# Kernel tuning notes

Measured on AMD Instinct MI355X. Metric: run time of the kernel, lower is better.

## Reference

```python
import jax, jax.numpy as jnp
import numpy as np

N_HEAD = 16
N_FEAT = 1024
HEAD_DIM = N_FEAT // N_HEAD


def setup_inputs() -> dict:
    key = jax.random.key(0)
    ks = jax.random.split(key, 13)
    B, Tq, Tc = 2, 1024, 1024
    s = 0.02
    return {
        "query": jax.random.normal(ks[0], (B, Tq, N_FEAT), jnp.float32),
        "key": jax.random.normal(ks[1], (B, Tq, N_FEAT), jnp.float32),
        "value": jax.random.normal(ks[2], (B, Tq, N_FEAT), jnp.float32),
        "cache": jax.random.normal(ks[3], (B, N_HEAD, Tc, 2 * HEAD_DIM), jnp.float32),
        "Wq": jax.random.normal(ks[4], (N_FEAT, N_FEAT), jnp.float32) * s,
        "bq": jax.random.normal(ks[5], (N_FEAT,), jnp.float32) * s,
        "Wk": jax.random.normal(ks[6], (N_FEAT, N_FEAT), jnp.float32) * s,
        "bk": jax.random.normal(ks[7], (N_FEAT,), jnp.float32) * s,
        "Wv": jax.random.normal(ks[8], (N_FEAT, N_FEAT), jnp.float32) * s,
        "bv": jax.random.normal(ks[9], (N_FEAT,), jnp.float32) * s,
        "Wo": jax.random.normal(ks[10], (N_FEAT, N_FEAT), jnp.float32) * s,
        "bo": jax.random.normal(ks[11], (N_FEAT,), jnp.float32) * s,
    }


def _split_heads(x, B):
    # [B, T, C] -> [B, H, T, D]
    return x.reshape(B, -1, N_HEAD, HEAD_DIM).transpose(0, 2, 1, 3)


def reference(query, key, value, cache, Wq, bq, Wk, bk, Wv, bv, Wo, bo):
    B, Tq, _ = query.shape
    # torch Linear: y = x @ W.T + b
    q = _split_heads(query @ Wq.T + bq, B)   # [B,H,Tq,D]
    k = _split_heads(key @ Wk.T + bk, B)     # [B,H,Tk,D]
    v = _split_heads(value @ Wv.T + bv, B)
    # KV-cache concat (cache holds [K | V] along last dim)
    k_cache, v_cache = jnp.split(cache, 2, axis=-1)
    k = jnp.concatenate([k_cache, k], axis=2)
    v = jnp.concatenate([v_cache, v], axis=2)
    new_cache = jnp.concatenate([k, v], axis=-1)
    scores = jnp.einsum("bhqd,bhkd->bhqk", q, k) / np.sqrt(HEAD_DIM).astype(jnp.float32)
    attn = jax.nn.softmax(scores, axis=-1)  # fake mask path; dropout is identity (rate 0 / eval)
    x = jnp.einsum("bhqk,bhkd->bhqd", attn, v)
    x = x.transpose(0, 2, 1, 3).reshape(B, Tq, N_FEAT)
    out = x @ Wo.T + bo
    return out, new_cache
```

## Files before the change

kernel.cpp:

```cpp
#include <hip/hip_runtime.h>

typedef short short4s __attribute__((ext_vector_type(4)));
typedef short short8 __attribute__((ext_vector_type(8)));
typedef __bf16 bf16x8 __attribute__((ext_vector_type(8)));
typedef float f32x4 __attribute__((ext_vector_type(4)));

#define NFEAT 1024
#define HDIM  64
#define NHEAD 16
#define TC2   2048
#define QSCL  0.18033688011112043f

__device__ __forceinline__ short f2bf(float f) {
    unsigned int u = __builtin_bit_cast(unsigned int, f);
    u += 0x7fffu + ((u >> 16) & 1u);
    return (short)(u >> 16);
}
__device__ __forceinline__ short f2bfq(float f) {
    __bf16 h = (__bf16)f;
    return __builtin_bit_cast(short, h);
}

__device__ __forceinline__ f32x4 mfma_bf16(short8 a, short8 b, f32x4 c) {
    return __builtin_amdgcn_mfma_f32_16x16x32_bf16(
        __builtin_bit_cast(bf16x8, a), __builtin_bit_cast(bf16x8, b), c, 0, 0, 0);
}

#define GLOAD16(gp, lp) __builtin_amdgcn_global_load_lds( \
    (const __attribute__((address_space(1))) void*)(gp),  \
    (__attribute__((address_space(3))) void*)(lp), 16, 0, 0)

__global__ __launch_bounds__(256) void prep_kernel(
    const float* __restrict__ q, const float* __restrict__ k, const float* __restrict__ v,
    const float* __restrict__ Wq, const float* __restrict__ Wk,
    const float* __restrict__ Wv, const float* __restrict__ Wo,
    const float4* __restrict__ cache4,
    short* __restrict__ qin, short* __restrict__ kin, short* __restrict__ vin,
    short* __restrict__ wqb, short* __restrict__ wkb, short* __restrict__ wvb,
    short* __restrict__ wob,
    float4* __restrict__ nc4, short* __restrict__ kbb, short* __restrict__ vtb)
{
    const int b = blockIdx.x, tid = threadIdx.x;
    if (b < 5120) {
        const float* src; short* dst; size_t base;
        if (b < 1024)      { src = q;  dst = qin; base = (size_t)b * 2048; }
        else if (b < 2048) { src = k;  dst = kin; base = (size_t)(b - 1024) * 2048; }
        else if (b < 3072) { src = v;  dst = vin; base = (size_t)(b - 2048) * 2048; }
        else if (b < 3584) { src = Wq; dst = wqb; base = (size_t)(b - 3072) * 2048; }
        else if (b < 4096) { src = Wk; dst = wkb; base = (size_t)(b - 3584) * 2048; }
        else if (b < 4608) { src = Wv; dst = wvb; base = (size_t)(b - 4096) * 2048; }
        else               { src = Wo; dst = wob; base = (size_t)(b - 4608) * 2048; }
        size_t i = base + (size_t)tid * 8;
        float4 a0 = *(const float4*)(src + i);
        float4 a1 = *(const float4*)(src + i + 4);
        short8 o;
        o[0] = f2bf(a0.x); o[1] = f2bf(a0.y); o[2] = f2bf(a0.z); o[3] = f2bf(a0.w);
        o[4] = f2bf(a1.x); o[5] = f2bf(a1.y); o[6] = f2bf(a1.z); o[7] = f2bf(a1.w);
        *(short8*)(dst + i) = o;
    } else {
        int i = (b - 5120) * 256 + tid;
        int c4 = i & 31;
        int t  = (i >> 5) & 1023;
        int bh = i >> 15;
        float4 val = cache4[i];
        nc4[((size_t)bh * TC2 + t) * 32 + c4] = val;
        int c = c4 * 4;
        if (c < 64) {
            size_t base = ((size_t)bh * TC2 + t) * HDIM + c;
            kbb[base + 0] = f2bf(val.x); kbb[base + 1] = f2bf(val.y);
            kbb[base + 2] = f2bf(val.z); kbb[base + 3] = f2bf(val.w);
        } else {
            int d = c - 64;
            size_t base = ((size_t)bh * HDIM + d) * TC2 + t;
            vtb[base + 0 * TC2] = f2bf(val.x); vtb[base + 1 * TC2] = f2bf(val.y);
            vtb[base + 2 * TC2] = f2bf(val.z); vtb[base + 3 * TC2] = f2bf(val.w);
        }
    }
}

__global__ __launch_bounds__(256) void gemm128(
    const short* __restrict__ A0, const short* __restrict__ A1, const short* __restrict__ A2,
    const short* __restrict__ W0, const short* __restrict__ W1, const short* __restrict__ W2,
    const float* __restrict__ b0, const float* __restrict__ b1, const float* __restrict__ b2,
    float* __restrict__ outf, short* __restrict__ qbuf,
    short* __restrict__ kbb, short* __restrict__ vtb, int base_mode)
{
    __shared__ short As[128 * 64];
    __shared__ short Bs[128 * 64];

    int mode;
    const short *A, *W;
    const float* bias;
    if (base_mode == 3) { mode = 3; A = A0; W = W0; bias = b0; }
    else {
        mode = blockIdx.z;
        if (mode == 0)      { A = A0; W = W0; bias = b0; }
        else if (mode == 1) { A = A1; W = W1; bias = b1; }
        else                { A = A2; W = W2; bias = b2; }
    }

    const int tid = threadIdx.x, lane = tid & 63, w = tid >> 6;
    const int wr = w >> 1, wc = w & 1;
    const int lr = lane & 15, lg = lane >> 4;
    const int bx = blockIdx.x, by = blockIdx.y;

    f32x4 acc[4][4];
#pragma unroll
    for (int m = 0; m < 4; ++m)
#pragma unroll
        for (int n = 0; n < 4; ++n) acc[m][n] = (f32x4){0.f, 0.f, 0.f, 0.f};

    const short* agBase = A + (size_t)(by * 128 + w * 32 + (lane >> 3)) * 1024 + (lane & 7) * 8;
    const short* bgBase = W + (size_t)(bx * 128 + w * 32 + (lane >> 3)) * 1024 + (lane & 7) * 8;
    short* asW = &As[w * 2048];
    short* bsW = &Bs[w * 2048];

    for (int kt = 0; kt < 16; ++kt) {
        const short* ag = agBase + kt * 64;
        const short* bg = bgBase + kt * 64;
        GLOAD16(ag,          asW);
        GLOAD16(ag + 8192,   asW + 512);
        GLOAD16(ag + 16384,  asW + 1024);
        GLOAD16(ag + 24576,  asW + 1536);
        GLOAD16(bg,          bsW);
        GLOAD16(bg + 8192,   bsW + 512);
        GLOAD16(bg + 16384,  bsW + 1024);
        GLOAD16(bg + 24576,  bsW + 1536);
        __syncthreads();
#pragma unroll
        for (int kk = 0; kk < 2; ++kk) {
            short8 af[4], bf[4];
#pragma unroll
            for (int m = 0; m < 4; ++m)
                af[m] = *(const short8*)&As[(wr * 64 + m * 16 + lr) * 64 + kk * 32 + lg * 8];
#pragma unroll
            for (int n = 0; n < 4; ++n)
                bf[n] = *(const short8*)&Bs[(wc * 64 + n * 16 + lr) * 64 + kk * 32 + lg * 8];
#pragma unroll
            for (int m = 0; m < 4; ++m)
#pragma unroll
                for (int n = 0; n < 4; ++n)
                    acc[m][n] = mfma_bf16(af[m], bf[n], acc[m][n]);
        }
        __syncthreads();
    }

#pragma unroll
    for (int m = 0; m < 4; ++m) {
#pragma unroll
        for (int n = 0; n < 4; ++n) {
            const int cg = bx * 128 + wc * 64 + n * 16 + lr;
            const int rg0 = by * 128 + wr * 64 + m * 16 + lg * 4;
            const float bv = bias[cg];
            if (mode == 3) {
#pragma unroll
                for (int r = 0; r < 4; ++r)
                    outf[(size_t)(rg0 + r) * NFEAT + cg] = acc[m][n][r] + bv;
            } else {
                const int b = rg0 >> 10, t0 = rg0 & 1023;
                const int h = cg >> 6, d = cg & 63;
                const size_t bh = (size_t)b * NHEAD + h;
                if (mode == 0) {
#pragma unroll
                    for (int r = 0; r < 4; ++r)
                        qbuf[(bh * 1024 + t0 + r) * HDIM + d] = f2bf((acc[m][n][r] + bv) * QSCL);
                } else if (mode == 1) {
#pragma unroll
                    for (int r = 0; r < 4; ++r) {
                        float val = acc[m][n][r] + bv;
                        outf[(bh * TC2 + 1024 + t0 + r) * 128 + d] = val;
                        kbb[(bh * TC2 + 1024 + t0 + r) * HDIM + d] = f2bf(val);
                    }
                } else {
                    short4s pk;
#pragma unroll
                    for (int r = 0; r < 4; ++r) {
                        float val = acc[m][n][r] + bv;
                        outf[(bh * TC2 + 1024 + t0 + r) * 128 + 64 + d] = val;
                        pk[r] = f2bf(val);
                    }
                    *(short4s*)&vtb[(bh * HDIM + d) * TC2 + 1024 + t0] = pk;
                }
            }
        }
    }
}

__global__ __launch_bounds__(256) void attn_kernel(
    const short* __restrict__ qb, const short* __restrict__ kb,
    const short* __restrict__ vtb, float* __restrict__ opart, float* __restrict__ mlbuf)
{
    __shared__ short Ks[2][64 * 64];
    __shared__ short Vs[2][64 * 64];
    __shared__ short Ps[4][16 * 64];

    const int tid = threadIdx.x, lane = tid & 63, w = tid >> 6;
    const int lr = lane & 15, lg = lane >> 4;
    const int b0 = blockIdx.x;
    const int xcd = b0 & 7, rest = b0 >> 3;
    const int qt = rest & 15, ghi = rest >> 4;
    const int g = ghi * 8 + xcd;
    const int bh = g >> 1, half = g & 1;
    const int xz = lr & 7;

    const short* qrow = qb + ((size_t)bh * 1024 + qt * 64 + w * 16 + lr) * HDIM + lg * 8;
    const short8 bq0 = *(const short8*)(qrow);
    const short8 bq1 = *(const short8*)(qrow + 32);

    const int rT = w * 16 + (lane >> 3);
    const int cswz = ((lane & 7) ^ (rT & 7)) * 8;
    const short* kgb = kb  + ((size_t)bh * TC2 + half * 1024 + rT) * HDIM + cswz;
    const short* vgb = vtb + ((size_t)bh * HDIM + rT) * TC2 + half * 1024 + cswz;
    short* kdst = &Ks[0][0] + w * 1024;
    short* vdst = &Vs[0][0] + w * 1024;

#define STAGE(bufsel, kvt_) do {                                         \
        const short* kg_ = kgb + (size_t)(kvt_) * 64 * HDIM;             \
        const short* vg_ = vgb + (kvt_) * 64;                            \
        GLOAD16(kg_,            kdst + (bufsel) * 4096);                 \
        GLOAD16(kg_ + 8 * HDIM, kdst + (bufsel) * 4096 + 512);           \
        GLOAD16(vg_,            vdst + (bufsel) * 4096);                 \
        GLOAD16(vg_ + 8 * TC2,  vdst + (bufsel) * 4096 + 512);           \
    } while (0)

    f32x4 accx[4];
#pragma unroll
    for (int i = 0; i < 4; ++i) accx[i] = (f32x4){0.f, 0.f, 0.f, 0.f};
    float ms = -3.0e38f, ls = 0.f;
    short* pw = &Ps[w][0];

    STAGE(0, 0);
    __syncthreads();

    int cur = 0;
    for (int kvt = 0; kvt < 16; ++kvt) {
        if (kvt < 15) STAGE(cur ^ 1, kvt + 1);
        const short* Kc = &Ks[cur][0];
        const short* Vc = &Vs[cur][0];

        f32x4 s[4];
#pragma unroll
        for (int n = 0; n < 4; ++n) {
            const short* kt = Kc + (n * 16 + lr) * 64;
            short8 k0 = *(const short8*)&kt[(lg ^ xz) * 8];
            short8 k1 = *(const short8*)&kt[((4 + lg) ^ xz) * 8];
            s[n] = (f32x4){0.f, 0.f, 0.f, 0.f};
            s[n] = mfma_bf16(k0, bq0, s[n]);
            s[n] = mfma_bf16(k1, bq1, s[n]);
        }

        float v8[8];
#pragma unroll
        for (int i = 0; i < 8; ++i) v8[i] = fmaxf(s[i >> 1][(i & 1) * 2], s[i >> 1][(i & 1) * 2 + 1]);
        float v4a = fmaxf(v8[0], v8[1]), v4b = fmaxf(v8[2], v8[3]);
        float v4c = fmaxf(v8[4], v8[5]), v4d = fmaxf(v8[6], v8[7]);
        float pmax = fmaxf(fmaxf(v4a, v4b), fmaxf(v4c, v4d));
        pmax = fmaxf(pmax, __shfl_xor(pmax, 16));
        pmax = fmaxf(pmax, __shfl_xor(pmax, 32));

        if (!__all(pmax - ms <= 8.0f)) {
            float mn = fmaxf(ms, pmax);
            float alpha = __builtin_amdgcn_exp2f(ms - mn);
            ms = mn;
            ls *= alpha;
            float ar[4];
#pragma unroll
            for (int r = 0; r < 4; ++r) ar[r] = __shfl(alpha, lg * 4 + r);
#pragma unroll
            for (int nd = 0; nd < 4; ++nd)
#pragma unroll
                for (int r = 0; r < 4; ++r) accx[nd][r] *= ar[r];
        }

        float p[4][4];
        float sm[8];
#pragma unroll
        for (int n = 0; n < 4; ++n)
#pragma unroll
            for (int r = 0; r < 4; ++r) p[n][r] = __builtin_amdgcn_exp2f(s[n][r] - ms);
#pragma unroll
        for (int i = 0; i < 8; ++i) sm[i] = p[i >> 1][(i & 1) * 2] + p[i >> 1][(i & 1) * 2 + 1];
        float rs = ((sm[0] + sm[1]) + (sm[2] + sm[3])) + ((sm[4] + sm[5]) + (sm[6] + sm[7]));
        rs += __shfl_xor(rs, 16);
        rs += __shfl_xor(rs, 32);
        ls += rs;

#pragma unroll
        for (int n = 0; n < 4; ++n) {
            short4s pk;
            pk[0] = f2bfq(p[n][0]); pk[1] = f2bfq(p[n][1]);
            pk[2] = f2bfq(p[n][2]); pk[3] = f2bfq(p[n][3]);
            int slot = (2 * n + (lg >> 1)) ^ xz;
            *(short4s*)&pw[lr * 64 + slot * 8 + (lg & 1) * 4] = pk;
        }

        short8 ap0 = *(const short8*)&pw[lr * 64 + (lg ^ xz) * 8];
        short8 ap1 = *(const short8*)&pw[lr * 64 + ((4 + lg) ^ xz) * 8];
#pragma unroll
        for (int nd = 0; nd < 4; ++nd) {
            const short* vt = Vc + (nd * 16 + lr) * 64;
            short8 vf0 = *(const short8*)&vt[(lg ^ xz) * 8];
            short8 vf1 = *(const short8*)&vt[((4 + lg) ^ xz) * 8];
            accx[nd] = mfma_bf16(ap0, vf0, accx[nd]);
            accx[nd] = mfma_bf16(ap1, vf1, accx[nd]);
        }

        __syncthreads();
        cur ^= 1;
    }

    const size_t rbase = (size_t)half * 32768 + (size_t)bh * 1024 + qt * 64 + w * 16;
#pragma unroll
    for (int nd = 0; nd < 4; ++nd)
#pragma unroll
        for (int r = 0; r < 4; ++r)
            opart[(rbase + lg * 4 + r) * 64 + nd * 16 + lr] = accx[nd][r];
    if (lg == 0) {
        mlbuf[(rbase + lr) * 2]     = ms;
        mlbuf[(rbase + lr) * 2 + 1] = ls;
    }
#undef STAGE
}

__global__ __launch_bounds__(256) void combine_kernel(
    const float* __restrict__ opart, const float* __restrict__ mlbuf,
    short* __restrict__ xb)
{
    int idx = blockIdx.x * 256 + threadIdx.x;
    int r = idx >> 3, d8 = (idx & 7) * 8;
    float m1 = mlbuf[r * 2],             l1 = mlbuf[r * 2 + 1];
    float m2 = mlbuf[(32768 + r) * 2],   l2 = mlbuf[(32768 + r) * 2 + 1];
    float M  = fmaxf(m1, m2);
    float w1 = __builtin_amdgcn_exp2f(m1 - M);
    float w2 = __builtin_amdgcn_exp2f(m2 - M);
    float inv = 1.0f / (l1 * w1 + l2 * w2);
    const float* o1 = opart + (size_t)r * 64 + d8;
    const float* o2 = opart + (size_t)(32768 + r) * 64 + d8;
    float4 a0 = *(const float4*)o1, a1 = *(const float4*)(o1 + 4);
    float4 b0 = *(const float4*)o2, b1 = *(const float4*)(o2 + 4);
    short8 o;
    o[0] = f2bfq((a0.x * w1 + b0.x * w2) * inv);
    o[1] = f2bfq((a0.y * w1 + b0.y * w2) * inv);
    o[2] = f2bfq((a0.z * w1 + b0.z * w2) * inv);
    o[3] = f2bfq((a0.w * w1 + b0.w * w2) * inv);
    o[4] = f2bfq((a1.x * w1 + b1.x * w2) * inv);
    o[5] = f2bfq((a1.y * w1 + b1.y * w2) * inv);
    o[6] = f2bfq((a1.z * w1 + b1.z * w2) * inv);
    o[7] = f2bfq((a1.w * w1 + b1.w * w2) * inv);
    int bh = r >> 10, tq = r & 1023;
    int b = bh >> 4, h = bh & 15;
    *(short8*)&xb[((size_t)(b * 1024 + tq)) * NFEAT + h * 64 + d8] = o;
}

extern "C" void kernel_launch(void* const* d_in, const int* in_sizes, int n_in,
                              void* d_out, int out_size, void* d_ws, size_t ws_size,
                              hipStream_t stream) {
    const float* query = (const float*)d_in[0];
    const float* key   = (const float*)d_in[1];
    const float* value = (const float*)d_in[2];
    const float* cache = (const float*)d_in[3];
    const float* Wq = (const float*)d_in[4];
    const float* bq = (const float*)d_in[5];
    const float* Wk = (const float*)d_in[6];
    const float* bk = (const float*)d_in[7];
    const float* Wv = (const float*)d_in[8];
    const float* bv = (const float*)d_in[9];
    const float* Wo = (const float*)d_in[10];
    const float* bo = (const float*)d_in[11];

    float* out0   = (float*)d_out;
    float* ncache = out0 + (size_t)2 * 1024 * 1024;

    short* qin = (short*)d_ws;
    short* kin = qin + (size_t)2097152;
    short* vin = kin + (size_t)2097152;
    short* wqb = vin + (size_t)2097152;
    short* wkb = wqb + (size_t)1048576;
    short* wvb = wkb + (size_t)1048576;
    short* wob = wvb + (size_t)1048576;
    short* qbuf = wob + (size_t)1048576;
    short* kbb  = qbuf + (size_t)2097152;
    short* vtb  = kbb  + (size_t)4194304;
    float* opart = (float*)d_ws;
    float* mlbuf = (float*)(qin + (size_t)8388608);
    short* xb    = qbuf;

    prep_kernel<<<9216, 256, 0, stream>>>(query, key, value, Wq, Wk, Wv, Wo,
        (const float4*)cache, qin, kin, vin, wqb, wkb, wvb, wob,
        (float4*)ncache, kbb, vtb);

    gemm128<<<dim3(8, 16, 3), 256, 0, stream>>>(qin, kin, vin, wqb, wkb, wvb,
        bq, bk, bv, ncache, qbuf, kbb, vtb, 0);

    attn_kernel<<<1024, 256, 0, stream>>>(qbuf, kbb, vtb, opart, mlbuf);

    combine_kernel<<<1024, 256, 0, stream>>>(opart, mlbuf, xb);

    gemm128<<<dim3(8, 16, 1), 256, 0, stream>>>(xb, nullptr, nullptr, wob, nullptr, nullptr,
        bo, nullptr, nullptr, out0, nullptr, nullptr, nullptr, 3);
}
```

Before: 121.4 us.

## Split attention KV into quarters with 512-thread blocks and bf16 partials

```diff
diff --git a/kernel.cpp b/kernel.cpp
--- a/kernel.cpp
+++ b/kernel.cpp
@@ -19,6 +19,10 @@
 __device__ __forceinline__ short f2bfq(float f) {
     __bf16 h = (__bf16)f;
     return __builtin_bit_cast(short, h);
+}
+__device__ __forceinline__ float bf2f(short s) {
+    unsigned int u = ((unsigned int)(unsigned short)s) << 16;
+    return __builtin_bit_cast(float, u);
 }
 
 __device__ __forceinline__ f32x4 mfma_bf16(short8 a, short8 b, f32x4 c) {
@@ -186,41 +190,39 @@
     }
 }
 
-__global__ __launch_bounds__(256) void attn_kernel(
+__global__ __launch_bounds__(512) void attn_kernel(
     const short* __restrict__ qb, const short* __restrict__ kb,
-    const short* __restrict__ vtb, float* __restrict__ opart, float* __restrict__ mlbuf)
+    const short* __restrict__ vtb, short* __restrict__ opart, float* __restrict__ mlbuf)
 {
     __shared__ short Ks[2][64 * 64];
     __shared__ short Vs[2][64 * 64];
-    __shared__ short Ps[4][16 * 64];
+    __shared__ short Ps[8][16 * 64];
 
     const int tid = threadIdx.x, lane = tid & 63, w = tid >> 6;
     const int lr = lane & 15, lg = lane >> 4;
     const int b0 = blockIdx.x;
     const int xcd = b0 & 7, rest = b0 >> 3;
-    const int qt = rest & 15, ghi = rest >> 4;
-    const int g = ghi * 8 + xcd;
-    const int bh = g >> 1, half = g & 1;
+    const int unit = xcd + 8 * (rest & 15);
+    const int qt = rest >> 4;
+    const int bh = unit >> 2, quarter = unit & 3;
     const int xz = lr & 7;
 
-    const short* qrow = qb + ((size_t)bh * 1024 + qt * 64 + w * 16 + lr) * HDIM + lg * 8;
+    const short* qrow = qb + ((size_t)bh * 1024 + qt * 128 + w * 16 + lr) * HDIM + lg * 8;
     const short8 bq0 = *(const short8*)(qrow);
     const short8 bq1 = *(const short8*)(qrow + 32);
 
-    const int rT = w * 16 + (lane >> 3);
-    const int cswz = ((lane & 7) ^ (rT & 7)) * 8;
-    const short* kgb = kb  + ((size_t)bh * TC2 + half * 1024 + rT) * HDIM + cswz;
-    const short* vgb = vtb + ((size_t)bh * HDIM + rT) * TC2 + half * 1024 + cswz;
-    short* kdst = &Ks[0][0] + w * 1024;
-    short* vdst = &Vs[0][0] + w * 1024;
+    const int srow = tid >> 3;
+    const int scx = ((tid & 7) ^ (srow & 7)) * 8;
+    const short* kgb = kb  + ((size_t)bh * TC2 + quarter * 512 + srow) * HDIM + scx;
+    const short* vgb = vtb + ((size_t)bh * HDIM + srow) * TC2 + quarter * 512 + scx;
+    short* kdst = &Ks[0][0] + w * 512;
+    short* vdst = &Vs[0][0] + w * 512;
 
 #define STAGE(bufsel, kvt_) do {                                         \
         const short* kg_ = kgb + (size_t)(kvt_) * 64 * HDIM;             \
         const short* vg_ = vgb + (kvt_) * 64;                            \
-        GLOAD16(kg_,            kdst + (bufsel) * 4096);                 \
-        GLOAD16(kg_ + 8 * HDIM, kdst + (bufsel) * 4096 + 512);           \
-        GLOAD16(vg_,            vdst + (bufsel) * 4096);                 \
-        GLOAD16(vg_ + 8 * TC2,  vdst + (bufsel) * 4096 + 512);           \
+        GLOAD16(kg_, kdst + (bufsel) * 4096);                            \
+        GLOAD16(vg_, vdst + (bufsel) * 4096);                            \
     } while (0)
 
     f32x4 accx[4];
@@ -233,8 +235,8 @@
     __syncthreads();
 
     int cur = 0;
-    for (int kvt = 0; kvt < 16; ++kvt) {
-        if (kvt < 15) STAGE(cur ^ 1, kvt + 1);
+    for (int kvt = 0; kvt < 8; ++kvt) {
+        if (kvt < 7) STAGE(cur ^ 1, kvt + 1);
         const short* Kc = &Ks[cur][0];
         const short* Vc = &Vs[cur][0];
 
@@ -309,12 +311,12 @@
         cur ^= 1;
     }
 
-    const size_t rbase = (size_t)half * 32768 + (size_t)bh * 1024 + qt * 64 + w * 16;
+    const size_t rbase = (size_t)quarter * 32768 + (size_t)bh * 1024 + qt * 128 + w * 16;
 #pragma unroll
     for (int nd = 0; nd < 4; ++nd)
 #pragma unroll
         for (int r = 0; r < 4; ++r)
-            opart[(rbase + lg * 4 + r) * 64 + nd * 16 + lr] = accx[nd][r];
+            opart[(rbase + lg * 4 + r) * 64 + nd * 16 + lr] = f2bfq(accx[nd][r]);
     if (lg == 0) {
         mlbuf[(rbase + lr) * 2]     = ms;
         mlbuf[(rbase + lr) * 2 + 1] = ls;
@@ -323,30 +325,34 @@
 }
 
 __global__ __launch_bounds__(256) void combine_kernel(
-    const float* __restrict__ opart, const float* __restrict__ mlbuf,
+    const short* __restrict__ opart, const float* __restrict__ mlbuf,
     short* __restrict__ xb)
 {
     int idx = blockIdx.x * 256 + threadIdx.x;
     int r = idx >> 3, d8 = (idx & 7) * 8;
-    float m1 = mlbuf[r * 2],             l1 = mlbuf[r * 2 + 1];
-    float m2 = mlbuf[(32768 + r) * 2],   l2 = mlbuf[(32768 + r) * 2 + 1];
-    float M  = fmaxf(m1, m2);
-    float w1 = __builtin_amdgcn_exp2f(m1 - M);
-    float w2 = __builtin_amdgcn_exp2f(m2 - M);
-    float inv = 1.0f / (l1 * w1 + l2 * w2);
-    const float* o1 = opart + (size_t)r * 64 + d8;
-    const float* o2 = opart + (size_t)(32768 + r) * 64 + d8;
-    float4 a0 = *(const float4*)o1, a1 = *(const float4*)(o1 + 4);
-    float4 b0 = *(const float4*)o2, b1 = *(const float4*)(o2 + 4);
+    float m[4], l[4];
+#pragma unroll
+    for (int i = 0; i < 4; ++i) {
+        m[i] = mlbuf[((size_t)i * 32768 + r) * 2];
+        l[i] = mlbuf[((size_t)i * 32768 + r) * 2 + 1];
+    }
+    float M = fmaxf(fmaxf(m[0], m[1]), fmaxf(m[2], m[3]));
+    float acc[8];
+#pragma unroll
+    for (int j = 0; j < 8; ++j) acc[j] = 0.f;
+    float lsum = 0.f;
+#pragma unroll
+    for (int i = 0; i < 4; ++i) {
+        float wi = __builtin_amdgcn_exp2f(m[i] - M);
+        lsum += l[i] * wi;
+        short8 op = *(const short8*)&opart[((size_t)i * 32768 + r) * 64 + d8];
+#pragma unroll
+        for (int j = 0; j < 8; ++j) acc[j] += bf2f(op[j]) * wi;
+    }
+    float inv = 1.0f / lsum;
     short8 o;
-    o[0] = f2bfq((a0.x * w1 + b0.x * w2) * inv);
-    o[1] = f2bfq((a0.y * w1 + b0.y * w2) * inv);
-    o[2] = f2bfq((a0.z * w1 + b0.z * w2) * inv);
-    o[3] = f2bfq((a0.w * w1 + b0.w * w2) * inv);
-    o[4] = f2bfq((a1.x * w1 + b1.x * w2) * inv);
-    o[5] = f2bfq((a1.y * w1 + b1.y * w2) * inv);
-    o[6] = f2bfq((a1.z * w1 + b1.z * w2) * inv);
-    o[7] = f2bfq((a1.w * w1 + b1.w * w2) * inv);
+#pragma unroll
+    for (int j = 0; j < 8; ++j) o[j] = f2bfq(acc[j] * inv);
     int bh = r >> 10, tq = r & 1023;
     int b = bh >> 4, h = bh & 15;
     *(short8*)&xb[((size_t)(b * 1024 + tq)) * NFEAT + h * 64 + d8] = o;
@@ -381,7 +387,7 @@
     short* qbuf = wob + (size_t)1048576;
     short* kbb  = qbuf + (size_t)2097152;
     short* vtb  = kbb  + (size_t)4194304;
-    float* opart = (float*)d_ws;
+    short* opart = (short*)d_ws;
     float* mlbuf = (float*)(qin + (size_t)8388608);
     short* xb    = qbuf;
 
@@ -392,7 +398,7 @@
     gemm128<<<dim3(8, 16, 3), 256, 0, stream>>>(qin, kin, vin, wqb, wkb, wvb,
         bq, bk, bv, ncache, qbuf, kbb, vtb, 0);
 
-    attn_kernel<<<1024, 256, 0, stream>>>(qbuf, kbb, vtb, opart, mlbuf);
+    attn_kernel<<<1024, 512, 0, stream>>>(qbuf, kbb, vtb, opart, mlbuf);
 
     combine_kernel<<<1024, 256, 0, stream>>>(opart, mlbuf, xb);
 
```

Measured after the change: 117.2 us. 3.5% less time.
